# Performance work log

Hardware: AMD Instinct MI355X
Metric: run time of the kernel (lower is better)

Reference implementation:

```python
import jax, jax.numpy as jnp
import numpy as np

N = 3072
R = 16
B = 16


def setup_inputs() -> dict:
    key = jax.random.key(0)
    k1, k2, k3, k4, k5 = jax.random.split(key, 5)
    z1 = jax.random.normal(k1, (N, R), dtype=jnp.float32)
    z2 = jax.random.normal(k2, (N, R), dtype=jnp.float32)
    seg_matrix = jax.random.randint(k3, (N, N), 0, 2).astype(jnp.float32)
    cls_label = jax.random.randint(k4, (N,), 0, 30).astype(jnp.int64)
    batch = jnp.sort(jax.random.randint(k5, (N,), 0, B)).astype(jnp.int64)
    return {"z1": z1, "z2": z2, "seg_matrix": seg_matrix,
            "cls_label": cls_label, "batch": batch}


def reference(z1, z2, seg_matrix, cls_label, batch):
    n, r = z1.shape
    # seg_matrix += eye(N): self-pairs never have seg == 0
    seg = seg_matrix + jnp.eye(n, dtype=seg_matrix.dtype)
    # nodes with class labels 24/25/26 are excluded
    node_mask = (cls_label != 24) & (cls_label != 25) & (cls_label != 26)
    # pair (i, j) is written iff both nodes valid, same graph, and seg[i,j] == 0.
    # (the per-batch meshgrid/nonzero loop == same-batch pair condition)
    pair = (node_mask[:, None] & node_mask[None, :]
            & (batch[:, None] == batch[None, :])
            & (seg == 0.0))                              # [N, N]
    # default value: one-hot on relation 0 (concat of ones and zeros)
    default = jax.nn.one_hot(0, r, dtype=z1.dtype)        # [R]
    prod = z1[:, None, :] * z2[None, :, :]                # [N, N, R]
    return jnp.where(pair[:, :, None], prod, default)
```

## Files before the change

### kernel.cpp

```cpp
#include <hip/hip_runtime.h>
#include <cstddef>

#define NN 3072
#define RR 16
#define NB 16
#define FILL_BLOCKS 64
#define FILL_ITERS 2304

typedef float f32x4 __attribute__((ext_vector_type(4)));

__global__ void frd_prep_kernel(const int* __restrict__ cls,
                                const int* __restrict__ batch,
                                int* __restrict__ key,
                                int* __restrict__ start) {
    int t = blockIdx.x * blockDim.x + threadIdx.x;
    if (t < NN) {
        int c = cls[t];
        int b = batch[t];
        key[t] = (c != 24 && c != 25 && c != 26) ? b : -1;
        int prev = (t == 0) ? -1 : batch[t - 1];
        for (int bb = prev + 1; bb <= b; ++bb) start[bb] = t;
        if (t == NN - 1)
            for (int bb = b + 1; bb <= NB; ++bb) start[bb] = NN;
    }
}

__global__ __launch_bounds__(256)
void frd_fill_kernel(float* __restrict__ out) {
    const int t = blockIdx.x * 256 + threadIdx.x;
    const float d0 = ((t & 3) == 0) ? 1.0f : 0.0f;
    const f32x4 r = {d0, 0.0f, 0.0f, 0.0f};
    float* p = out + (size_t)t * 4;
    const size_t step = (size_t)FILL_BLOCKS * 256 * 4;
#pragma unroll 8
    for (int it = 0; it < FILL_ITERS; ++it) {
        __builtin_nontemporal_store(r, reinterpret_cast<f32x4*>(p));
        p += step;
    }
}

__global__ __launch_bounds__(256)
void frd_diag_kernel(const float* __restrict__ z1,
                     const float* __restrict__ z2,
                     const float* __restrict__ seg,
                     const int* __restrict__ key,
                     const int* __restrict__ start,
                     float* __restrict__ out) {
    const int i = blockIdx.x;
    const int ki = key[i];
    if (ki < 0) return;
    const int s0 = start[ki];
    const int s1 = start[ki + 1];
    const int q = threadIdx.x & 3;
    const int g = threadIdx.x >> 2;

    const float4 a = *reinterpret_cast<const float4*>(z1 + i * RR + q * 4);

    for (int j = s0 + g; j < s1; j += 64) {
        if (key[j] != ki) continue;
        const float s = seg[i * NN + j];
        const float seg_eff = s + ((i == j) ? 1.0f : 0.0f);
        if (seg_eff != 0.0f) continue;
        const float4 b = *reinterpret_cast<const float4*>(z2 + j * RR + q * 4);
        f32x4 r;
        r.x = a.x * b.x; r.y = a.y * b.y; r.z = a.z * b.z; r.w = a.w * b.w;
        float* op = out + ((size_t)i * NN + j) * RR + q * 4;
        __builtin_nontemporal_store(r, reinterpret_cast<f32x4*>(op));
    }
}

extern "C" void kernel_launch(void* const* d_in, const int* in_sizes, int n_in,
                              void* d_out, int out_size, void* d_ws, size_t ws_size,
                              hipStream_t stream) {
    const float* z1  = (const float*)d_in[0];
    const float* z2  = (const float*)d_in[1];
    const float* seg = (const float*)d_in[2];
    const int* cls   = (const int*)d_in[3];
    const int* batch = (const int*)d_in[4];
    float* out = (float*)d_out;
    int* key   = (int*)d_ws;
    int* start = key + NN;

    frd_fill_kernel<<<FILL_BLOCKS, 256, 0, stream>>>(out);
    frd_prep_kernel<<<(NN + 255) / 256, 256, 0, stream>>>(cls, batch, key, start);
    frd_diag_kernel<<<NN, 256, 0, stream>>>(z1, z2, seg, key, start, out);
}
```

Measured before the change: 106.3 us.

## Skip default fill over same-batch block; diag kernel writes defaults there

The fill kernel now runs after prep and, for each valid row, skips the same-batch column range [start[k], start[k+1]). The diag kernel writes either the product or the one-hot default for every column in that range, so each output element is written exactly once. This removes the double write of roughly 1/16 of the output. In exchange, the fill loop becomes row-wise with variable bounds, and it now depends on prep finishing first.

New measurement: 122.9 us. 15.7% more time.

```diff
diff --git a/kernel.cpp b/kernel.cpp
--- a/kernel.cpp
+++ b/kernel.cpp
@@ -5,7 +5,6 @@
 #define RR 16
 #define NB 16
 #define FILL_BLOCKS 64
-#define FILL_ITERS 2304
 
 typedef float f32x4 __attribute__((ext_vector_type(4)));
 
@@ -26,16 +25,26 @@
 }
 
 __global__ __launch_bounds__(256)
-void frd_fill_kernel(float* __restrict__ out) {
-    const int t = blockIdx.x * 256 + threadIdx.x;
-    const float d0 = ((t & 3) == 0) ? 1.0f : 0.0f;
+void frd_fill_kernel(const int* __restrict__ key,
+                     const int* __restrict__ start,
+                     float* __restrict__ out) {
+    const int tid = threadIdx.x;
+    const float d0 = ((tid & 3) == 0) ? 1.0f : 0.0f;
     const f32x4 r = {d0, 0.0f, 0.0f, 0.0f};
-    float* p = out + (size_t)t * 4;
-    const size_t step = (size_t)FILL_BLOCKS * 256 * 4;
-#pragma unroll 8
-    for (int it = 0; it < FILL_ITERS; ++it) {
-        __builtin_nontemporal_store(r, reinterpret_cast<f32x4*>(p));
-        p += step;
+    const int rowquads = NN * 4;
+
+    for (int i = blockIdx.x; i < NN; i += FILL_BLOCKS) {
+        const int ki = key[i];
+        int e0 = rowquads, b1 = rowquads;
+        if (ki >= 0) {
+            e0 = start[ki] * 4;
+            b1 = start[ki + 1] * 4;
+        }
+        float* rowp = out + (size_t)i * NN * RR;
+        for (int q = tid; q < e0; q += 256)
+            __builtin_nontemporal_store(r, reinterpret_cast<f32x4*>(rowp + (size_t)q * 4));
+        for (int q = b1 + tid; q < rowquads; q += 256)
+            __builtin_nontemporal_store(r, reinterpret_cast<f32x4*>(rowp + (size_t)q * 4));
     }
 }
 
@@ -55,15 +64,18 @@
     const int g = threadIdx.x >> 2;
 
     const float4 a = *reinterpret_cast<const float4*>(z1 + i * RR + q * 4);
+    const float d0 = (q == 0) ? 1.0f : 0.0f;
 
     for (int j = s0 + g; j < s1; j += 64) {
-        if (key[j] != ki) continue;
-        const float s = seg[i * NN + j];
-        const float seg_eff = s + ((i == j) ? 1.0f : 0.0f);
-        if (seg_eff != 0.0f) continue;
-        const float4 b = *reinterpret_cast<const float4*>(z2 + j * RR + q * 4);
-        f32x4 r;
-        r.x = a.x * b.x; r.y = a.y * b.y; r.z = a.z * b.z; r.w = a.w * b.w;
+        f32x4 r = {d0, 0.0f, 0.0f, 0.0f};
+        if (key[j] == ki) {
+            const float s = seg[i * NN + j];
+            const float seg_eff = s + ((i == j) ? 1.0f : 0.0f);
+            if (seg_eff == 0.0f) {
+                const float4 b = *reinterpret_cast<const float4*>(z2 + j * RR + q * 4);
+                r.x = a.x * b.x; r.y = a.y * b.y; r.z = a.z * b.z; r.w = a.w * b.w;
+            }
+        }
         float* op = out + ((size_t)i * NN + j) * RR + q * 4;
         __builtin_nontemporal_store(r, reinterpret_cast<f32x4*>(op));
     }
@@ -81,7 +93,7 @@
     int* key   = (int*)d_ws;
     int* start = key + NN;
 
-    frd_fill_kernel<<<FILL_BLOCKS, 256, 0, stream>>>(out);
     frd_prep_kernel<<<(NN + 255) / 256, 256, 0, stream>>>(cls, batch, key, start);
+    frd_fill_kernel<<<FILL_BLOCKS, 256, 0, stream>>>(key, start, out);
     frd_diag_kernel<<<NN, 256, 0, stream>>>(z1, z2, seg, key, start, out);
 }
```
